# Kernel optimization log

Measured on AMD Instinct MI355X. Metric: run time of the kernel, lower is better.

The kernel has to match this reference:

```python
import jax, jax.numpy as jnp
from jax import lax
import numpy as np

# dims
VOCAB = 64
B, L = 64, 2048
EMB = 128
D_MODEL = 128
N_LAYERS = 4
D_INNER = 256      # expand=2
D_STATE = 16
D_CONV = 4
DT_RANK = 8        # ceil(d_model/16)
NCLS = 3
BN_EPS = 1e-5
RMS_EPS = 1e-5


def setup_inputs():
    key = jax.random.key(0)
    ks = iter(jax.random.split(key, 48))
    def rn(shape, s=0.02):
        return jax.random.normal(next(ks), shape, jnp.float32) * s
    tokens = jax.random.randint(next(ks), (B, L), 0, VOCAB)
    mask = jnp.ones((B, L), jnp.float32)
    emb = rn((VOCAB, EMB)).at[0].set(0.0)  # padding_idx=0
    bn_w = jnp.ones((EMB,), jnp.float32)
    bn_b = jnp.zeros((EMB,), jnp.float32)
    conv_w = rn((D_MODEL, EMB, 3))
    conv_b = jnp.zeros((D_MODEL,), jnp.float32)
    in_proj_w = rn((N_LAYERS, 2 * D_INNER, D_MODEL))
    conv1d_w = rn((N_LAYERS, D_INNER, D_CONV), 0.1)
    conv1d_b = jnp.zeros((N_LAYERS, D_INNER), jnp.float32)
    x_proj_w = rn((N_LAYERS, DT_RANK + 2 * D_STATE, D_INNER))
    dt_proj_w = rn((N_LAYERS, D_INNER, DT_RANK), 0.1)
    dt_proj_b = rn((N_LAYERS, D_INNER), 0.1)
    A_log = jnp.tile(jnp.log(jnp.arange(1, D_STATE + 1, dtype=jnp.float32))[None, None, :],
                     (N_LAYERS, D_INNER, 1))
    D_param = jnp.ones((N_LAYERS, D_INNER), jnp.float32)
    out_proj_w = rn((N_LAYERS, D_MODEL, D_INNER))
    norm_w = jnp.ones((N_LAYERS, D_MODEL), jnp.float32)
    lin1_w = rn((512, D_MODEL)); lin1_b = jnp.zeros((512,), jnp.float32)
    lin2_w = rn((512, 512));     lin2_b = jnp.zeros((512,), jnp.float32)
    lin3_w = rn((NCLS, 512));    lin3_b = jnp.zeros((NCLS,), jnp.float32)
    return dict(tokens=tokens, mask=mask, emb=emb, bn_w=bn_w, bn_b=bn_b,
                conv_w=conv_w, conv_b=conv_b, in_proj_w=in_proj_w,
                conv1d_w=conv1d_w, conv1d_b=conv1d_b, x_proj_w=x_proj_w,
                dt_proj_w=dt_proj_w, dt_proj_b=dt_proj_b, A_log=A_log,
                D_param=D_param, out_proj_w=out_proj_w, norm_w=norm_w,
                lin1_w=lin1_w, lin1_b=lin1_b, lin2_w=lin2_w, lin2_b=lin2_b,
                lin3_w=lin3_w, lin3_b=lin3_b)


def _rmsnorm(x, w):
    return x * lax.rsqrt(jnp.mean(x * x, axis=-1, keepdims=True) + RMS_EPS) * w


def _selective_scan(u, dt, A, Bm, Cm, Dv):
    # u, dt: (B,L,di); A: (di,ds); Bm, Cm: (B,L,ds); Dv: (di,)
    def step(h, inp):
        dt_t, B_t, C_t, u_t = inp           # (B,di),(B,ds),(B,ds),(B,di)
        dA = jnp.exp(dt_t[:, :, None] * A)  # (B,di,ds)
        h = dA * h + (dt_t * u_t)[:, :, None] * B_t[:, None, :]
        y = jnp.einsum('bds,bs->bd', h, C_t)
        return h, y
    h0 = jnp.zeros((u.shape[0], A.shape[0], A.shape[1]), u.dtype)
    xs = (jnp.swapaxes(dt, 0, 1), jnp.swapaxes(Bm, 0, 1),
          jnp.swapaxes(Cm, 0, 1), jnp.swapaxes(u, 0, 1))
    _, ys = lax.scan(step, h0, xs)          # ys: (L,B,di)
    return jnp.swapaxes(ys, 0, 1) + u * Dv


def _mamba(x, in_w, cw, cb, xp_w, dtp_w, dtp_b, A_log, Dv, out_w):
    # x: (B,L,d_model)
    xz = jnp.einsum('bld,ed->ble', x, in_w)            # (B,L,2*di)
    xi, z = jnp.split(xz, 2, axis=-1)
    # causal depthwise conv over time
    xc = jnp.swapaxes(xi, 1, 2)                        # (B,di,L)
    xc = lax.conv_general_dilated(xc, cw[:, None, :], (1,), [(D_CONV - 1, 0)],
                                  dimension_numbers=('NCH', 'OIH', 'NCH'),
                                  feature_group_count=D_INNER)
    xc = jax.nn.silu(xc + cb[None, :, None])
    xc = jnp.swapaxes(xc, 1, 2)                        # (B,L,di)
    x_dbl = jnp.einsum('bld,ed->ble', xc, xp_w)        # (B,L,dtr+2*ds)
    dt = jax.nn.softplus(jnp.einsum('blr,dr->bld', x_dbl[..., :DT_RANK], dtp_w) + dtp_b)
    Bm = x_dbl[..., DT_RANK:DT_RANK + D_STATE]
    Cm = x_dbl[..., DT_RANK + D_STATE:]
    A = -jnp.exp(A_log)                                # (di,ds)
    y = _selective_scan(xc, dt, A, Bm, Cm, Dv)
    y = y * jax.nn.silu(z)
    return jnp.einsum('ble,de->bld', y, out_w)         # (B,L,d_model)


def _forward(tokens, mask, emb, bn_w, bn_b, conv_w, conv_b, in_proj_w,
             conv1d_w, conv1d_b, x_proj_w, dt_proj_w, dt_proj_b, A_log,
             D_param, out_proj_w, norm_w, lin1_w, lin1_b, lin2_w, lin2_b,
             lin3_w, lin3_b):
    x = emb[tokens]                                    # (B,L,E)
    xc = jnp.swapaxes(x, 1, 2)                         # (B,E,L)
    # BatchNorm1d in eval mode: running_mean=0, running_var=1
    xc = xc * (bn_w * lax.rsqrt(jnp.array(1.0 + BN_EPS)))[None, :, None] + bn_b[None, :, None]
    xc = lax.conv_general_dilated(xc, conv_w, (1,), [(1, 1)],
                                  dimension_numbers=('NCH', 'OIH', 'NCH'))
    xc = jax.nn.relu(xc + conv_b[None, :, None])
    x = jnp.swapaxes(xc, 1, 2)                         # (B,L,D_MODEL)
    for i in range(N_LAYERS):
        x = _mamba(_rmsnorm(x, norm_w[i]), in_proj_w[i], conv1d_w[i],
                   conv1d_b[i], x_proj_w[i], dt_proj_w[i], dt_proj_b[i],
                   A_log[i], D_param[i], out_proj_w[i]) + x
    # masked average pooling
    m = mask[:, :, None]
    denom = jnp.clip(jnp.sum(m, axis=1), 1e-9, None)   # (B,1)->(B,D) broadcast
    pooled = jnp.sum(x * m, axis=1) / denom
    h = jax.nn.relu(pooled @ lin1_w.T + lin1_b)
    h = jax.nn.relu(h @ lin2_w.T + lin2_b)
    return h @ lin3_w.T + lin3_b                       # (B,NCLS)


def reference(tokens, mask, emb, bn_w, bn_b, conv_w, conv_b, in_proj_w,
              conv1d_w, conv1d_b, x_proj_w, dt_proj_w, dt_proj_b, A_log,
              D_param, out_proj_w, norm_w, lin1_w, lin1_b, lin2_w, lin2_b,
              lin3_w, lin3_b):
    return _forward(tokens, mask, emb, bn_w, bn_b, conv_w, conv_b, in_proj_w,
                    conv1d_w, conv1d_b, x_proj_w, dt_proj_w, dt_proj_b, A_log,
                    D_param, out_proj_w, norm_w, lin1_w, lin1_b, lin2_w,
                    lin2_b, lin3_w, lin3_b)
```

## Files before the change

### kernel.cpp

```cpp
#include <hip/hip_runtime.h>
#include <math.h>

#define NB     64
#define SL     2048
#define NTOK   (NB*SL)
#define EMB_D  128
#define DMODEL 128
#define DIN    256
#define DST    16
#define NLAYER 4
#define SEG    64
#define NSEG   (SL/SEG)
#define L2E    1.4426950408889634f
#define LN2    0.6931471805599453f

typedef __bf16 bf16x8 __attribute__((ext_vector_type(8)));
typedef __bf16 bf16x4 __attribute__((ext_vector_type(4)));
typedef float  f32x4  __attribute__((ext_vector_type(4)));
typedef float  f32x2  __attribute__((ext_vector_type(2)));

#define FIX_PL   ((size_t)0)
#define FIX_PM   (FIX_PL + 131072)
#define FIX_PD   (FIX_PM + 1024)
#define FIX_H1   (FIX_PD + 8192)
#define FIX_H2   (FIX_H1 + 32768)
#define FIX_WP   (FIX_H2 + 32768)
#define FIX_W2B  (FIX_WP + 65536)
#define FIX_WINB (FIX_W2B + 24576)
#define FIX_WOUTB (FIX_WINB + 131072)
#define FIX_END  (FIX_WOUTB + 65536)

__device__ __forceinline__ float fexp2(float x){ return __builtin_amdgcn_exp2f(x); }
__device__ __forceinline__ float flog2(float x){ return __builtin_amdgcn_logf(x); }
__device__ __forceinline__ float frcp (float x){ return __builtin_amdgcn_rcpf(x); }
__device__ __forceinline__ float fast_exp(float x){ return fexp2(x*L2E); }
__device__ __forceinline__ float siluf(float v){ return v * frcp(1.f + fast_exp(-v)); }
__device__ __forceinline__ float softplusf(float a){
  return fmaxf(a,0.f) + flog2(1.f + fexp2(-fabsf(a)*L2E)) * LN2;
}
__device__ __forceinline__ unsigned short bfbits(float x){
  __bf16 b = (__bf16)x; return __builtin_bit_cast(unsigned short, b);
}
__device__ __forceinline__ unsigned int packdu(float dt, float u){
  return ((unsigned int)bfbits(u) << 16) | (unsigned int)bfbits(dt);
}

__device__ __forceinline__ f32x2 pkfma(f32x2 a, f32x2 b, f32x2 c){
#if __has_builtin(__builtin_elementwise_fma)
  return __builtin_elementwise_fma(a, b, c);
#else
  return (f32x2){ fmaf(a.x,b.x,c.x), fmaf(a.y,b.y,c.y) };
#endif
}

__global__ void k_w2b(const float* __restrict__ cw, __bf16* __restrict__ w2){
  int g = blockIdx.x*256 + threadIdx.x;
  if (g >= 128*384) return;
  int d = g / 384, j = g % 384;
  int k = j >> 7, e = j & 127;
  w2[d*384 + k*128 + e] = (__bf16)cw[d*384 + e*3 + k];
}

__global__ void k_cvt(const float* __restrict__ src, __bf16* __restrict__ dst, int n){
  int i = blockIdx.x*256 + threadIdx.x;
  if (i < n) dst[i] = (__bf16)src[i];
}

__global__ void k_wprep(const float* __restrict__ xpw, __bf16* __restrict__ wp){
  int g = blockIdx.x*256 + threadIdx.x;
  int l = g >> 14, rem = g & 16383;
  int n = rem >> 8, k = rem & 255;
  float v = (n < 40) ? xpw[(size_t)l*40*256 + n*256 + k] : 0.f;
  wp[g] = (__bf16)v;
}

__global__ __launch_bounds__(256) void k_rmsscale(const float* __restrict__ x,
                                                  float* __restrict__ rs){
  int wv = threadIdx.x>>6, lane = threadIdx.x&63;
  size_t tok = (size_t)blockIdx.x*4 + wv;
  float2 v = *(const float2*)(x + tok*128 + lane*2);
  float ss = v.x*v.x + v.y*v.y;
  #pragma unroll
  for (int m=1;m<64;m<<=1) ss += __shfl_xor(ss, m);
  float r = rsqrtf(ss*(1.f/128.f) + 1e-5f);
  if (lane == 0) rs[tok] = r;
}

template<int MODE, int K, int N>
__global__ __launch_bounds__(256) void k_mgemm(
    const void* __restrict__ Av, const __bf16* __restrict__ Wb,
    const float* __restrict__ bias, const float* __restrict__ rsp,
    const float* __restrict__ nwp, const float* __restrict__ bnbp,
    float* __restrict__ out, __bf16* __restrict__ outb, __bf16* __restrict__ outz){
  __shared__ __bf16 As[128][40];
  __shared__ __bf16 Bs[128][40];
  const int tid  = threadIdx.x;
  const int wave = tid >> 6;
  const int lane = tid & 63;
  const int col  = lane & 15;
  const int quad = lane >> 4;
  const int wm = (wave & 1) * 64;
  const int wn = (wave >> 1) * 64;
  const int m0 = blockIdx.y * 128;
  const int n0 = blockIdx.x * 128;

  f32x4 acc[4][4];
  #pragma unroll
  for (int i=0;i<4;i++)
    #pragma unroll
    for (int j=0;j<4;j++) acc[i][j] = (f32x4){0.f,0.f,0.f,0.f};

  const int sm = tid >> 3;
  const int sk4 = (tid & 7) * 4;
  const int bn = tid >> 2;
  const int bk8 = (tid & 3) * 8;

  for (int k0 = 0; k0 < K; k0 += 32){
    if constexpr(MODE==0){
      const int* tok = (const int*)Av;
      const int tap = k0 >> 7;
      const int e = (k0 & 127) + sk4;
      const float sc = rsqrtf(1.0f + 1e-5f);
      float4 bw4 = *(const float4*)(nwp + e);
      float4 bb4 = *(const float4*)(bnbp + e);
      float4 s4;
      s4.x = bw4.x*sc; s4.y = bw4.y*sc; s4.z = bw4.z*sc; s4.w = bw4.w*sc;
      #pragma unroll
      for (int p=0;p<4;p++){
        int m = p*32 + sm;
        int tokpos = m0 + m;
        int t = (tokpos & 2047) + tap - 1;
        float4 v = {0.f,0.f,0.f,0.f};
        if ((unsigned)t < 2048u){
          int id = tok[((size_t)(tokpos >> 11) << 11) + t];
          float4 ev = *(const float4*)(rsp + (size_t)id*EMB_D + e);
          v.x = fmaf(ev.x, s4.x, bb4.x);
          v.y = fmaf(ev.y, s4.y, bb4.y);
          v.z = fmaf(ev.z, s4.z, bb4.z);
          v.w = fmaf(ev.w, s4.w, bb4.w);
        }
        bf16x4 o;
        o[0] = (__bf16)v.x; o[1] = (__bf16)v.y; o[2] = (__bf16)v.z; o[3] = (__bf16)v.w;
        *(bf16x4*)&As[m][sk4] = o;
      }
    } else {
      const size_t abase = (size_t)m0 * K;
      #pragma unroll
      for (int p=0;p<4;p++){
        int m = p*32 + sm;
        const float* A = (const float*)Av;
        float4 x4 = *(const float4*)(A + abase + (size_t)m*K + k0 + sk4);
        float4 w4 = *(const float4*)(nwp + k0 + sk4);
        float s = rsp[m0 + m];
        float4 v;
        v.x = x4.x*s*w4.x; v.y = x4.y*s*w4.y; v.z = x4.z*s*w4.z; v.w = x4.w*s*w4.w;
        bf16x4 o;
        o[0] = (__bf16)v.x; o[1] = (__bf16)v.y; o[2] = (__bf16)v.z; o[3] = (__bf16)v.w;
        *(bf16x4*)&As[m][sk4] = o;
      }
    }
    #pragma unroll
    for (int p=0;p<2;p++){
      int n = p*64 + bn;
      bf16x8 w = *(const bf16x8*)(Wb + (size_t)(n0+n)*K + k0 + bk8);
      *(bf16x8*)&Bs[n][bk8] = w;
    }
    __syncthreads();
    bf16x8 af[4], bfr[4];
    const int fq = quad*8;
    #pragma unroll
    for (int i=0;i<4;i++) af[i]  = *(const bf16x8*)&As[wm + i*16 + col][fq];
    #pragma unroll
    for (int j=0;j<4;j++) bfr[j] = *(const bf16x8*)&Bs[wn + j*16 + col][fq];
    #pragma unroll
    for (int i=0;i<4;i++)
      #pragma unroll
      for (int j=0;j<4;j++)
        acc[i][j] = __builtin_amdgcn_mfma_f32_16x16x32_bf16(af[i], bfr[j], acc[i][j], 0, 0, 0);
    __syncthreads();
  }

  #pragma unroll
  for (int i=0;i<4;i++){
    #pragma unroll
    for (int j=0;j<4;j++){
      int n_l = wn + j*16 + col;
      #pragma unroll
      for (int r=0;r<4;r++){
        int m = m0 + wm + i*16 + quad*4 + r;
        float c = acc[i][j][r];
        if constexpr(MODE==0){
          int n = n0 + n_l;
          out[(size_t)m*DMODEL + n] = fmaxf(c + bias[n], 0.f);
        } else {
          int n = n0 + n_l;
          if (n < DIN) outb[(size_t)m*DIN + n]        = (__bf16)c;
          else         outz[(size_t)m*DIN + n - DIN]  = (__bf16)siluf(c);
        }
      }
    }
  }
}

__global__ __launch_bounds__(256) void k_seg(const __bf16* __restrict__ xi,
    const __bf16* __restrict__ wpb,
    const float* __restrict__ cw, const float* __restrict__ cb,
    const float* __restrict__ dtw, const float* __restrict__ dtb,
    const float* __restrict__ alog,
    float* __restrict__ vbc, unsigned int* __restrict__ dub,
    float* __restrict__ cseg, float* __restrict__ sdtb){
  __shared__ __bf16 sxc[64][264];
  __shared__ float vls[64][68];
  const int tid = threadIdx.x;
  const size_t m0 = (size_t)blockIdx.x * 64;
  const int b = (int)(m0 >> 11);
  const int g = (int)((m0 >> 6) & (NSEG-1));
  const int seq0 = (int)(m0 & 2047);

  {
    const int c4 = (tid & 63) * 4;
    const int tw = tid >> 6;
    const int t0 = tw * 16;
    float wc[4][4];
    #pragma unroll
    for (int j=0;j<4;j++)
      #pragma unroll
      for (int k=0;k<4;k++) wc[j][k] = cw[(c4+j)*4 + k];
    float4 cb4 = *(const float4*)(cb + c4);
    bf16x4 zed;
    zed[0] = (__bf16)0.f; zed[1] = (__bf16)0.f; zed[2] = (__bf16)0.f; zed[3] = (__bf16)0.f;
    bf16x4 win[3];
    #pragma unroll
    for (int j=0;j<3;j++){
      int tr = t0 - 3 + j;
      win[j] = (seq0 + tr >= 0) ? *(const bf16x4*)(xi + (m0 + tr)*DIN + c4) : zed;
    }
    #pragma unroll
    for (int i=0;i<16;i++){
      int t = t0 + i;
      bf16x4 w3 = *(const bf16x4*)(xi + (m0 + t)*DIN + c4);
      float4 acc = cb4;
      #pragma unroll
      for (int k=0;k<3;k++){
        acc.x = fmaf(wc[0][k], (float)win[k][0], acc.x);
        acc.y = fmaf(wc[1][k], (float)win[k][1], acc.y);
        acc.z = fmaf(wc[2][k], (float)win[k][2], acc.z);
        acc.w = fmaf(wc[3][k], (float)win[k][3], acc.w);
      }
      acc.x = fmaf(wc[0][3], (float)w3[0], acc.x);
      acc.y = fmaf(wc[1][3], (float)w3[1], acc.y);
      acc.z = fmaf(wc[2][3], (float)w3[2], acc.z);
      acc.w = fmaf(wc[3][3], (float)w3[3], acc.w);
      bf16x4 o;
      o[0]=(__bf16)siluf(acc.x); o[1]=(__bf16)siluf(acc.y);
      o[2]=(__bf16)siluf(acc.z); o[3]=(__bf16)siluf(acc.w);
      *(bf16x4*)&sxc[t][c4] = o;
      win[0] = win[1]; win[1] = win[2]; win[2] = w3;
    }
  }
  __syncthreads();

  {
    const int wave = tid >> 6, lane = tid & 63;
    const int col = lane & 15, quad = lane >> 4;
    const int wn = wave * 16;
    f32x4 acc[4];
    #pragma unroll
    for (int i=0;i<4;i++) acc[i] = (f32x4){0.f,0.f,0.f,0.f};
    #pragma unroll
    for (int kc=0;kc<8;kc++){
      bf16x8 bfr = *(const bf16x8*)(wpb + (size_t)(wn+col)*256 + kc*32 + quad*8);
      #pragma unroll
      for (int mi=0;mi<4;mi++){
        bf16x8 af = *(const bf16x8*)&sxc[mi*16 + col][kc*32 + quad*8];
        acc[mi] = __builtin_amdgcn_mfma_f32_16x16x32_bf16(af, bfr, acc[mi], 0, 0, 0);
      }
    }
    #pragma unroll
    for (int mi=0;mi<4;mi++)
      #pragma unroll
      for (int r=0;r<4;r++)
        vls[mi*16 + quad*4 + r][wn + col] = acc[mi][r];
  }
  __syncthreads();

  #pragma unroll
  for (int p=0;p<8;p++){
    int j = p*256 + tid;
    int t = j >> 5, i = j & 31;
    vbc[(m0+t)*32 + i] = vls[t][8+i];
  }

  {
    const int d = tid;
    const float a0 = -fast_exp(alog[d*DST]) * L2E;
    bool fast = true;
    for (int s=1;s<16;s++){
      float as = -fast_exp(alog[d*DST + s]) * L2E;
      fast = fast && (fabsf(as - (float)(s+1)*a0) <= 1e-3f*fabsf(as));
    }
    float4 w8a = *(const float4*)(dtw + d*8);
    float4 w8b = *(const float4*)(dtw + d*8 + 4);
    const f32x2 wA0 = {w8a.x, w8a.y}, wA1 = {w8a.z, w8a.w};
    const f32x2 wB0 = {w8b.x, w8b.y}, wB1 = {w8b.z, w8b.w};
    const float bd = dtb[d];
    float ssum = 0.f;
    size_t base = (((size_t)b*NSEG + g)*DIN + d)*DST;
    if (fast){
      f32x2 hp[8];
      #pragma unroll
      for (int k=0;k<8;k++) hp[k] = (f32x2){0.f,0.f};
      float4 cv0 = *(const float4*)&vls[0][0];
      float4 cv1 = *(const float4*)&vls[0][4];
      float4 cb0 = *(const float4*)&vls[0][8];
      float4 cb1 = *(const float4*)&vls[0][12];
      float4 cb2 = *(const float4*)&vls[0][16];
      float4 cb3 = *(const float4*)&vls[0][20];
      float cu = (float)sxc[0][d];
      #pragma unroll 2
      for (int t=0;t<SEG;t++){
        float4 v0=cv0, v1=cv1, b0=cb0, b1=cb1, b2=cb2, b3=cb3;
        float u = cu;
        int tn = (t < SEG-1) ? t+1 : SEG-1;
        cv0 = *(const float4*)&vls[tn][0];
        cv1 = *(const float4*)&vls[tn][4];
        cb0 = *(const float4*)&vls[tn][8];
        cb1 = *(const float4*)&vls[tn][12];
        cb2 = *(const float4*)&vls[tn][16];
        cb3 = *(const float4*)&vls[tn][20];
        cu = (float)sxc[tn][d];
        f32x2 la = pkfma((f32x2){v0.x,v0.y}, wA0, (f32x2){bd, 0.f});
        la = pkfma((f32x2){v0.z,v0.w}, wA1, la);
        la = pkfma((f32x2){v1.x,v1.y}, wB0, la);
        la = pkfma((f32x2){v1.z,v1.w}, wB1, la);
        float dt = softplusf(la.x + la.y);
        ssum += dt;
        dub[(m0+t)*DIN + d] = packdu(dt, u);
        float du = dt*u;
        float r1 = fexp2(dt*a0);
        float r2 = r1*r1, r4 = r2*r2, r8 = r4*r4;
        f32x2 p01 = {r1, r2};
        f32x2 s2 = {r2, r2}, s4 = {r4, r4}, s8 = {r8, r8};
        f32x2 p23 = p01*s2, p45 = p01*s4, p67 = p23*s4;
        f32x2 p89 = p01*s8, pAB = p23*s8, pCD = p45*s8, pEF = p67*s8;
        f32x2 du2 = {du, du};
        hp[0] = pkfma(p01, hp[0], du2*(f32x2){b0.x,b0.y});
        hp[1] = pkfma(p23, hp[1], du2*(f32x2){b0.z,b0.w});
        hp[2] = pkfma(p45, hp[2], du2*(f32x2){b1.x,b1.y});
        hp[3] = pkfma(p67, hp[3], du2*(f32x2){b1.z,b1.w});
        hp[4] = pkfma(p89, hp[4], du2*(f32x2){b2.x,b2.y});
        hp[5] = pkfma(pAB, hp[5], du2*(f32x2){b2.z,b2.w});
        hp[6] = pkfma(pCD, hp[6], du2*(f32x2){b3.x,b3.y});
        hp[7] = pkfma(pEF, hp[7], du2*(f32x2){b3.z,b3.w});
      }
      #pragma unroll
      for (int k=0;k<4;k++){
        float4 o = { hp[2*k].x, hp[2*k].y, hp[2*k+1].x, hp[2*k+1].y };
        *(float4*)(cseg + base + 4*k) = o;
      }
    } else {
      float h[16];
      float aA[16];
      #pragma unroll
      for (int k=0;k<16;k++){ h[k] = 0.f; aA[k] = -fast_exp(alog[d*DST + k]) * L2E; }
      for (int t=0;t<SEG;t++){
        float4 v0 = *(const float4*)&vls[t][0];
        float4 v1 = *(const float4*)&vls[t][4];
        float lin = bd;
        lin = fmaf(v0.x,w8a.x, fmaf(v0.y,w8a.y, fmaf(v0.z,w8a.z, fmaf(v0.w,w8a.w, lin))));
        lin = fmaf(v1.x,w8b.x, fmaf(v1.y,w8b.y, fmaf(v1.z,w8b.z, fmaf(v1.w,w8b.w, lin))));
        float dt = softplusf(lin);
        ssum += dt;
        float u = (float)sxc[t][d];
        dub[(m0+t)*DIN + d] = packdu(dt, u);
        float du = dt*u;
        #pragma unroll
        for (int k=0;k<16;k++){
          float e = fexp2(dt*aA[k]);
          h[k] = fmaf(e, h[k], du*vls[t][8+k]);
        }
      }
      #pragma unroll
      for (int k=0;k<4;k++){
        float4 o = { h[4*k], h[4*k+1], h[4*k+2], h[4*k+3] };
        *(float4*)(cseg + base + 4*k) = o;
      }
    }
    sdtb[((size_t)b*NSEG + g)*DIN + d] = ssum;
  }
}

__global__ __launch_bounds__(256) void k_scanB(float* __restrict__ cseg,
    const float* __restrict__ sdtb, const float* __restrict__ alog){
  int gl = blockIdx.x*256 + threadIdx.x;
  int b   = gl >> 12;
  int rem = gl & 4095;
  int d = rem >> 4, s = rem & 15;
  const float a = -fast_exp(alog[d*DST + s]) * L2E;
  float cvals[NSEG];
  float sdv[NSEG];
  #pragma unroll
  for (int g=0; g<NSEG; g++){
    size_t base = ((size_t)b*NSEG + g)*DIN;
    sdv[g]   = sdtb[base + d];
    cvals[g] = cseg[(base + d)*DST + s];
  }
  float h = 0.f;
  #pragma unroll
  for (int g=0; g<NSEG; g++){
    size_t ci = (((size_t)b*NSEG + g)*DIN + d)*DST + s;
    cseg[ci] = h;
    h = fmaf(fexp2(a*sdv[g]), h, cvals[g]);
  }
}

__global__ __launch_bounds__(256) void k_scanC3(float* __restrict__ xres,
    const unsigned int* __restrict__ dub, const float* __restrict__ vbc,
    const __bf16* __restrict__ gzb,
    const float* __restrict__ alog, const float* __restrict__ Dpar,
    const float* __restrict__ cseg, const __bf16* __restrict__ wout,
    float* __restrict__ rs){
  __shared__ __bf16 sy[64][264];
  __shared__ float svbc[64][32];
  float* sx = (float*)sy;
  const int tid = threadIdx.x;
  const size_t m0 = (size_t)blockIdx.x * 64;
  const int b = (int)(m0 >> 11);
  const int g = (int)((m0 >> 6) & (NSEG-1));

  #pragma unroll
  for (int p=0;p<8;p++){
    int j = p*256 + tid;
    int t = j >> 5, i = j & 31;
    svbc[t][i] = vbc[(m0+t)*32 + i];
  }

  {
    const int d = tid;
    const float a0 = -fast_exp(alog[d*DST]) * L2E;
    bool fast = true;
    for (int s=1;s<16;s++){
      float as = -fast_exp(alog[d*DST + s]) * L2E;
      fast = fast && (fabsf(as - (float)(s+1)*a0) <= 1e-3f*fabsf(as));
    }
    const float Dv = Dpar[d];
    size_t base = (((size_t)b*NSEG + g)*DIN + d)*DST;
    float4 hv0 = *(const float4*)(cseg + base);
    float4 hv1 = *(const float4*)(cseg + base + 4);
    float4 hv2 = *(const float4*)(cseg + base + 8);
    float4 hv3 = *(const float4*)(cseg + base + 12);
    __syncthreads();

    if (fast){
      f32x2 hp[8] = { {hv0.x,hv0.y},{hv0.z,hv0.w},{hv1.x,hv1.y},{hv1.z,hv1.w},
                      {hv2.x,hv2.y},{hv2.z,hv2.w},{hv3.x,hv3.y},{hv3.z,hv3.w} };

#define LOADCH(WV,GV,T0) \
      _Pragma("unroll") \
      for (int q=0;q<8;q++){ \
        WV[q] = dub[(m0 + (T0) + q)*DIN + d]; \
        GV[q] = gzb[(m0 + (T0) + q)*DIN + d]; \
      }

#define SCSTEP(T,WW,GG) { \
      int Tn = ((T) < SEG-1) ? (T)+1 : SEG-1; \
      float4 nb0 = *(const float4*)&svbc[Tn][0]; \
      float4 nb1 = *(const float4*)&svbc[Tn][4]; \
      float4 nb2 = *(const float4*)&svbc[Tn][8]; \
      float4 nb3 = *(const float4*)&svbc[Tn][12]; \
      float4 nb4 = *(const float4*)&svbc[Tn][16]; \
      float4 nb5 = *(const float4*)&svbc[Tn][20]; \
      float4 nb6 = *(const float4*)&svbc[Tn][24]; \
      float4 nb7 = *(const float4*)&svbc[Tn][28]; \
      float u  = __builtin_bit_cast(float, (WW) & 0xffff0000u); \
      float dt = __builtin_bit_cast(float, (WW) << 16); \
      float du = dt*u; \
      float r1 = fexp2(dt*a0); \
      float r2 = r1*r1, r4 = r2*r2, r8 = r4*r4; \
      f32x2 p01 = {r1, r2}; \
      f32x2 s2 = {r2, r2}, s4 = {r4, r4}, s8 = {r8, r8}; \
      f32x2 p23 = p01*s2, p45 = p01*s4, p67 = p23*s4; \
      f32x2 p89 = p01*s8, pAB = p23*s8, pCD = p45*s8, pEF = p67*s8; \
      f32x2 du2 = {du, du}; \
      f32x2 ya = {0.f,0.f}, yb = {0.f,0.f}; \
      hp[0] = pkfma(p01, hp[0], du2*(f32x2){pb0.x,pb0.y}); \
      ya = pkfma(hp[0], (f32x2){pb4.x,pb4.y}, ya); \
      hp[1] = pkfma(p23, hp[1], du2*(f32x2){pb0.z,pb0.w}); \
      yb = pkfma(hp[1], (f32x2){pb4.z,pb4.w}, yb); \
      hp[2] = pkfma(p45, hp[2], du2*(f32x2){pb1.x,pb1.y}); \
      ya = pkfma(hp[2], (f32x2){pb5.x,pb5.y}, ya); \
      hp[3] = pkfma(p67, hp[3], du2*(f32x2){pb1.z,pb1.w}); \
      yb = pkfma(hp[3], (f32x2){pb5.z,pb5.w}, yb); \
      hp[4] = pkfma(p89, hp[4], du2*(f32x2){pb2.x,pb2.y}); \
      ya = pkfma(hp[4], (f32x2){pb6.x,pb6.y}, ya); \
      hp[5] = pkfma(pAB, hp[5], du2*(f32x2){pb2.z,pb2.w}); \
      yb = pkfma(hp[5], (f32x2){pb6.z,pb6.w}, yb); \
      hp[6] = pkfma(pCD, hp[6], du2*(f32x2){pb3.x,pb3.y}); \
      ya = pkfma(hp[6], (f32x2){pb7.x,pb7.y}, ya); \
      hp[7] = pkfma(pEF, hp[7], du2*(f32x2){pb3.z,pb3.w}); \
      yb = pkfma(hp[7], (f32x2){pb7.z,pb7.w}, yb); \
      f32x2 ys = ya + yb; \
      float y = ys.x + ys.y; \
      sy[T][d] = (__bf16)((y + u*Dv) * (float)(GG)); \
      pb0=nb0; pb1=nb1; pb2=nb2; pb3=nb3; pb4=nb4; pb5=nb5; pb6=nb6; pb7=nb7; }

      unsigned int wv0[8], wv1[8];
      __bf16 gv0[8], gv1[8];
      LOADCH(wv0, gv0, 0)
      float4 pb0 = *(const float4*)&svbc[0][0];
      float4 pb1 = *(const float4*)&svbc[0][4];
      float4 pb2 = *(const float4*)&svbc[0][8];
      float4 pb3 = *(const float4*)&svbc[0][12];
      float4 pb4 = *(const float4*)&svbc[0][16];
      float4 pb5 = *(const float4*)&svbc[0][20];
      float4 pb6 = *(const float4*)&svbc[0][24];
      float4 pb7 = *(const float4*)&svbc[0][28];
      #pragma unroll
      for (int tc=0; tc<SEG; tc+=16){
        LOADCH(wv1, gv1, tc+8)
        #pragma unroll
        for (int q=0;q<8;q++){ SCSTEP(tc+q, wv0[q], gv0[q]) }
        if (tc+16 < SEG){ LOADCH(wv0, gv0, tc+16) }
        #pragma unroll
        for (int q=0;q<8;q++){ SCSTEP(tc+8+q, wv1[q], gv1[q]) }
      }
#undef LOADCH
#undef SCSTEP
    } else {
      float h[16] = {hv0.x,hv0.y,hv0.z,hv0.w, hv1.x,hv1.y,hv1.z,hv1.w,
                     hv2.x,hv2.y,hv2.z,hv2.w, hv3.x,hv3.y,hv3.z,hv3.w};
      float aA[16];
      #pragma unroll
      for (int k=0;k<16;k++) aA[k] = -fast_exp(alog[d*DST + k]) * L2E;
      for (int t=0;t<SEG;t++){
        unsigned int w = dub[(m0+t)*DIN + d];
        float u  = __builtin_bit_cast(float, w & 0xffff0000u);
        float dt = __builtin_bit_cast(float, w << 16);
        float du = dt*u;
        float y = 0.f;
        #pragma unroll
        for (int k=0;k<16;k++){
          float e = fexp2(dt*aA[k]);
          h[k] = fmaf(e, h[k], du*svbc[t][k]);
          y = fmaf(h[k], svbc[t][16+k], y);
        }
        float gz = (float)gzb[(m0+t)*DIN + d];
        sy[t][d] = (__bf16)((y + u*Dv) * gz);
      }
    }
  }
  __syncthreads();

  const int wave = tid >> 6, lane = tid & 63;
  const int col = lane & 15, quad = lane >> 4;
  const int wn = wave * 32;
  f32x4 acc[4][2];
  #pragma unroll
  for (int i=0;i<4;i++)
    #pragma unroll
    for (int j=0;j<2;j++) acc[i][j] = (f32x4){0.f,0.f,0.f,0.f};
  #pragma unroll
  for (int kc=0;kc<8;kc++){
    bf16x8 bfr0 = *(const bf16x8*)(wout + (size_t)(wn +      col)*256 + kc*32 + quad*8);
    bf16x8 bfr1 = *(const bf16x8*)(wout + (size_t)(wn + 16 + col)*256 + kc*32 + quad*8);
    #pragma unroll
    for (int mi=0;mi<4;mi++){
      bf16x8 af = *(const bf16x8*)&sy[mi*16 + col][kc*32 + quad*8];
      acc[mi][0] = __builtin_amdgcn_mfma_f32_16x16x32_bf16(af, bfr0, acc[mi][0], 0, 0, 0);
      acc[mi][1] = __builtin_amdgcn_mfma_f32_16x16x32_bf16(af, bfr1, acc[mi][1], 0, 0, 0);
    }
  }
  __syncthreads();

  #pragma unroll
  for (int mi=0;mi<4;mi++){
    #pragma unroll
    for (int j=0;j<2;j++){
      int n = wn + j*16 + col;
      #pragma unroll
      for (int r=0;r<4;r++){
        int ml = mi*16 + quad*4 + r;
        size_t go = (m0 + ml)*DMODEL + n;
        float nx = xres[go] + acc[mi][j][r];
        xres[go] = nx;
        sx[ml*132 + n] = nx;
      }
    }
  }
  __syncthreads();
  {
    int row = tid >> 2, q = tid & 3;
    const float* pr = sx + row*132 + q*32;
    float ss = 0.f;
    #pragma unroll
    for (int i=0;i<32;i+=4){
      float4 v = *(const float4*)(pr + i);
      ss += v.x*v.x + v.y*v.y + v.z*v.z + v.w*v.w;
    }
    ss += __shfl_xor(ss, 1);
    ss += __shfl_xor(ss, 2);
    if (q == 0) rs[m0 + row] = rsqrtf(ss*(1.f/128.f) + 1e-5f);
  }
}

__global__ __launch_bounds__(256) void k_pool1(const float* __restrict__ x,
    const float* __restrict__ mask, float* __restrict__ part, float* __restrict__ pmask){
  int b = blockIdx.y, seg = blockIdx.x;
  int d = threadIdx.x & 127, half = threadIdx.x >> 7;
  int t0 = seg*128 + half*64;
  float acc = 0.f, macc = 0.f;
  for (int i=0;i<64;i++){
    int t = t0 + i;
    float mv = mask[(size_t)b*SL + t];
    acc = fmaf(x[((size_t)b*SL + t)*DMODEL + d], mv, acc);
    macc += mv;
  }
  __shared__ float sm[256];
  __shared__ float smm[2];
  sm[threadIdx.x] = acc;
  if (d == 0) smm[half] = macc;
  __syncthreads();
  if (half == 0){
    part[((size_t)b*16 + seg)*128 + d] = sm[d] + sm[128+d];
    if (d == 0) pmask[b*16 + seg] = smm[0] + smm[1];
  }
}

__global__ __launch_bounds__(512) void k_head(const float* __restrict__ part,
    const float* __restrict__ pmask,
    const float* __restrict__ l1w, const float* __restrict__ l1b,
    const float* __restrict__ l2w, const float* __restrict__ l2b,
    const float* __restrict__ l3w, const float* __restrict__ l3b,
    float* __restrict__ out){
  __shared__ float sp[128];
  __shared__ float sh[512];
  int b = blockIdx.x, tid = threadIdx.x;
  if (tid < 128){
    float acc = 0.f, ms = 0.f;
    for (int s=0;s<16;s++){
      acc += part[((size_t)b*16+s)*128 + tid];
      ms  += pmask[b*16+s];
    }
    sp[tid] = acc / fmaxf(ms, 1e-9f);
  }
  __syncthreads();
  {
    const float4* pw = (const float4*)(l1w + (size_t)tid*128);
    const float4* pi = (const float4*)sp;
    float acc = 0.f;
    #pragma unroll 8
    for (int k=0;k<32;k++){
      float4 a = pi[k], w = pw[k];
      acc = fmaf(a.x,w.x, fmaf(a.y,w.y, fmaf(a.z,w.z, fmaf(a.w,w.w, acc))));
    }
    __syncthreads();
    sh[tid] = fmaxf(acc + l1b[tid], 0.f);
  }
  __syncthreads();
  float h2v;
  {
    const float4* pw = (const float4*)(l2w + (size_t)tid*512);
    const float4* pi = (const float4*)sh;
    float acc = 0.f;
    #pragma unroll 8
    for (int k=0;k<128;k++){
      float4 a = pi[k], w = pw[k];
      acc = fmaf(a.x,w.x, fmaf(a.y,w.y, fmaf(a.z,w.z, fmaf(a.w,w.w, acc))));
    }
    h2v = fmaxf(acc + l2b[tid], 0.f);
  }
  __syncthreads();
  sh[tid] = h2v;
  __syncthreads();
  if (tid < 192){
    int n = tid >> 6, lane = tid & 63;
    float acc = 0.f;
    for (int k=lane; k<512; k+=64) acc = fmaf(sh[k], l3w[(size_t)n*512+k], acc);
    #pragma unroll
    for (int m=1;m<64;m<<=1) acc += __shfl_xor(acc, m);
    if (lane == 0) out[(size_t)b*3 + n] = acc + l3b[n];
  }
}

extern "C" void kernel_launch(void* const* d_in, const int* in_sizes, int n_in,
                              void* d_out, int out_size, void* d_ws, size_t ws_size,
                              hipStream_t stream){
  const int*   tokens = (const int*)  d_in[0];
  const float* mask   = (const float*)d_in[1];
  const float* emb    = (const float*)d_in[2];
  const float* bn_w   = (const float*)d_in[3];
  const float* bn_b   = (const float*)d_in[4];
  const float* conv_w = (const float*)d_in[5];
  const float* conv_b = (const float*)d_in[6];
  const float* in_w   = (const float*)d_in[7];
  const float* c1_w   = (const float*)d_in[8];
  const float* c1_b   = (const float*)d_in[9];
  const float* xp_w   = (const float*)d_in[10];
  const float* dtp_w  = (const float*)d_in[11];
  const float* dtp_b  = (const float*)d_in[12];
  const float* A_log  = (const float*)d_in[13];
  const float* D_par  = (const float*)d_in[14];
  const float* out_w  = (const float*)d_in[15];
  const float* nrm_w  = (const float*)d_in[16];
  const float* l1w = (const float*)d_in[17]; const float* l1b = (const float*)d_in[18];
  const float* l2w = (const float*)d_in[19]; const float* l2b = (const float*)d_in[20];
  const float* l3w = (const float*)d_in[21]; const float* l3b = (const float*)d_in[22];
  float* dout = (float*)d_out;

  int CB = 64;
  while (CB > 1 && ((size_t)CB*SL*741 + FIX_END)*4 > ws_size) CB >>= 1;
  if (((size_t)CB*SL*741 + FIX_END)*4 > ws_size) return;
  const size_t CTOK = (size_t)CB*SL;

  float* ws  = (float*)d_ws;
  float* pl  = ws + FIX_PL;
  float* pm  = ws + FIX_PM;
  __bf16* wpb   = (__bf16*)(ws + FIX_WP);
  __bf16* w2b   = (__bf16*)(ws + FIX_W2B);
  __bf16* winb  = (__bf16*)(ws + FIX_WINB);
  __bf16* woutb = (__bf16*)(ws + FIX_WOUTB);
  float* xcb = ws + FIX_END;
  float* rs  = xcb + CTOK*128;
  __bf16* xib = (__bf16*)(rs + CTOK);
  unsigned int* dub = (unsigned int*)(xib + CTOK*256);
  float* vbc = (float*)(dub + CTOK*256);
  float* csg = vbc + CTOK*32;
  float* sdt = csg + CTOK*64;
  __bf16* zb  = (__bf16*)(sdt + CTOK*4);

  k_w2b<<<192, 256, 0, stream>>>(conv_w, w2b);
  k_cvt<<<1024, 256, 0, stream>>>(in_w,  winb,  4*512*128);
  k_cvt<<<512,  256, 0, stream>>>(out_w, woutb, 4*128*256);
  k_wprep<<<256, 256, 0, stream>>>(xp_w, wpb);

  const int nchunks = NB / CB;
  for (int c = 0; c < nchunks; c++){
    const int* tok_c = tokens + (size_t)c*CTOK;

    k_mgemm<0,384,128><<<dim3(1, CTOK/128), 256, 0, stream>>>(
        tok_c, w2b, conv_b, emb, bn_w, bn_b, xcb, nullptr, nullptr);
    k_rmsscale<<<CTOK/4, 256, 0, stream>>>(xcb, rs);

    for (int layer = 0; layer < NLAYER; layer++){
      const __bf16* lin = winb  + (size_t)layer*512*128;
      const float* lcw  = c1_w  + (size_t)layer*DIN*4;
      const float* lcb  = c1_b  + (size_t)layer*DIN;
      const float* ldw  = dtp_w + (size_t)layer*DIN*8;
      const float* ldb  = dtp_b + (size_t)layer*DIN;
      const float* lal  = A_log + (size_t)layer*DIN*DST;
      const float* lD   = D_par + (size_t)layer*DIN;
      const __bf16* low = woutb + (size_t)layer*128*256;
      const float* lnw  = nrm_w + (size_t)layer*128;

      k_mgemm<1,128,512><<<dim3(4, CTOK/128), 256, 0, stream>>>(
          xcb, lin, nullptr, rs, lnw, nullptr, nullptr, xib, zb);
      k_seg<<<(int)(CTOK/64), 256, 0, stream>>>(
          xib, wpb + (size_t)layer*64*256, lcw, lcb, ldw, ldb, lal, vbc, dub, csg, sdt);
      k_scanB<<<CB*16, 256, 0, stream>>>(csg, sdt, lal);
      k_scanC3<<<(int)(CTOK/64), 256, 0, stream>>>(
          xcb, dub, vbc, zb, lal, lD, csg, low, rs);
    }

    k_pool1<<<dim3(16, CB), 256, 0, stream>>>(
        xcb, mask + (size_t)c*CTOK, pl + (size_t)c*CB*16*128, pm + (size_t)c*CB*16);
  }

  k_head<<<NB, 512, 0, stream>>>(pl, pm, l1w, l1b, l2w, l2b, l3w, l3b, dout);
}
```

Baseline: 1.348 ms.

## Split chunked scan output into intra-segment and carried-state parts across kernels

The segment kernel now computes the intra-segment output contribution (C·h from a zero start plus D·u) during its local scan and packs it in bf16 alongside dt. The final kernel then only adds the carried-in state's contribution, using a cumulative-dt decay, instead of re-running the full recurrence. This removes the duplicate recurrence in the final pass and halves the B/C buffer traffic, since only C is stored. The cost is extra work in the first pass and storing the partial output in bf16 rather than u, which may lose precision.

```diff
diff --git a/kernel.cpp b/kernel.cpp
--- a/kernel.cpp
+++ b/kernel.cpp
@@ -41,8 +41,8 @@
 __device__ __forceinline__ unsigned short bfbits(float x){
   __bf16 b = (__bf16)x; return __builtin_bit_cast(unsigned short, b);
 }
-__device__ __forceinline__ unsigned int packdu(float dt, float u){
-  return ((unsigned int)bfbits(u) << 16) | (unsigned int)bfbits(dt);
+__device__ __forceinline__ unsigned int packdu(float dt, float hi){
+  return ((unsigned int)bfbits(hi) << 16) | (unsigned int)bfbits(dt);
 }
 
 __device__ __forceinline__ f32x2 pkfma(f32x2 a, f32x2 b, f32x2 c){
@@ -206,7 +206,7 @@
     const __bf16* __restrict__ wpb,
     const float* __restrict__ cw, const float* __restrict__ cb,
     const float* __restrict__ dtw, const float* __restrict__ dtb,
-    const float* __restrict__ alog,
+    const float* __restrict__ alog, const float* __restrict__ Dpar,
     float* __restrict__ vbc, unsigned int* __restrict__ dub,
     float* __restrict__ cseg, float* __restrict__ sdtb){
   __shared__ __bf16 sxc[64][264];
@@ -285,10 +285,10 @@
   __syncthreads();
 
   #pragma unroll
-  for (int p=0;p<8;p++){
+  for (int p=0;p<4;p++){
     int j = p*256 + tid;
-    int t = j >> 5, i = j & 31;
-    vbc[(m0+t)*32 + i] = vls[t][8+i];
+    int t = j >> 4, i = j & 15;
+    vbc[(m0+t)*16 + i] = vls[t][24+i];
   }
 
   {
@@ -304,6 +304,7 @@
     const f32x2 wA0 = {w8a.x, w8a.y}, wA1 = {w8a.z, w8a.w};
     const f32x2 wB0 = {w8b.x, w8b.y}, wB1 = {w8b.z, w8b.w};
     const float bd = dtb[d];
+    const float Dv = Dpar[d];
     float ssum = 0.f;
     size_t base = (((size_t)b*NSEG + g)*DIN + d)*DST;
     if (fast){
@@ -312,22 +313,32 @@
       for (int k=0;k<8;k++) hp[k] = (f32x2){0.f,0.f};
       float4 cv0 = *(const float4*)&vls[0][0];
       float4 cv1 = *(const float4*)&vls[0][4];
-      float4 cb0 = *(const float4*)&vls[0][8];
-      float4 cb1 = *(const float4*)&vls[0][12];
-      float4 cb2 = *(const float4*)&vls[0][16];
-      float4 cb3 = *(const float4*)&vls[0][20];
+      float4 cbb0 = *(const float4*)&vls[0][8];
+      float4 cbb1 = *(const float4*)&vls[0][12];
+      float4 cbb2 = *(const float4*)&vls[0][16];
+      float4 cbb3 = *(const float4*)&vls[0][20];
+      float4 ccc0 = *(const float4*)&vls[0][24];
+      float4 ccc1 = *(const float4*)&vls[0][28];
+      float4 ccc2 = *(const float4*)&vls[0][32];
+      float4 ccc3 = *(const float4*)&vls[0][36];
       float cu = (float)sxc[0][d];
       #pragma unroll 2
       for (int t=0;t<SEG;t++){
-        float4 v0=cv0, v1=cv1, b0=cb0, b1=cb1, b2=cb2, b3=cb3;
+        float4 v0=cv0, v1=cv1;
+        float4 b0=cbb0, b1=cbb1, b2=cbb2, b3=cbb3;
+        float4 c0=ccc0, c1=ccc1, c2=ccc2, c3=ccc3;
         float u = cu;
         int tn = (t < SEG-1) ? t+1 : SEG-1;
         cv0 = *(const float4*)&vls[tn][0];
         cv1 = *(const float4*)&vls[tn][4];
-        cb0 = *(const float4*)&vls[tn][8];
-        cb1 = *(const float4*)&vls[tn][12];
-        cb2 = *(const float4*)&vls[tn][16];
-        cb3 = *(const float4*)&vls[tn][20];
+        cbb0 = *(const float4*)&vls[tn][8];
+        cbb1 = *(const float4*)&vls[tn][12];
+        cbb2 = *(const float4*)&vls[tn][16];
+        cbb3 = *(const float4*)&vls[tn][20];
+        ccc0 = *(const float4*)&vls[tn][24];
+        ccc1 = *(const float4*)&vls[tn][28];
+        ccc2 = *(const float4*)&vls[tn][32];
+        ccc3 = *(const float4*)&vls[tn][36];
         cu = (float)sxc[tn][d];
         f32x2 la = pkfma((f32x2){v0.x,v0.y}, wA0, (f32x2){bd, 0.f});
         la = pkfma((f32x2){v0.z,v0.w}, wA1, la);
@@ -335,7 +346,6 @@
         la = pkfma((f32x2){v1.z,v1.w}, wB1, la);
         float dt = softplusf(la.x + la.y);
         ssum += dt;
-        dub[(m0+t)*DIN + d] = packdu(dt, u);
         float du = dt*u;
         float r1 = fexp2(dt*a0);
         float r2 = r1*r1, r4 = r2*r2, r8 = r4*r4;
@@ -344,14 +354,26 @@
         f32x2 p23 = p01*s2, p45 = p01*s4, p67 = p23*s4;
         f32x2 p89 = p01*s8, pAB = p23*s8, pCD = p45*s8, pEF = p67*s8;
         f32x2 du2 = {du, du};
+        f32x2 ya = {0.f,0.f}, yb = {0.f,0.f};
         hp[0] = pkfma(p01, hp[0], du2*(f32x2){b0.x,b0.y});
+        ya = pkfma(hp[0], (f32x2){c0.x,c0.y}, ya);
         hp[1] = pkfma(p23, hp[1], du2*(f32x2){b0.z,b0.w});
+        yb = pkfma(hp[1], (f32x2){c0.z,c0.w}, yb);
         hp[2] = pkfma(p45, hp[2], du2*(f32x2){b1.x,b1.y});
+        ya = pkfma(hp[2], (f32x2){c1.x,c1.y}, ya);
         hp[3] = pkfma(p67, hp[3], du2*(f32x2){b1.z,b1.w});
+        yb = pkfma(hp[3], (f32x2){c1.z,c1.w}, yb);
         hp[4] = pkfma(p89, hp[4], du2*(f32x2){b2.x,b2.y});
+        ya = pkfma(hp[4], (f32x2){c2.x,c2.y}, ya);
         hp[5] = pkfma(pAB, hp[5], du2*(f32x2){b2.z,b2.w});
+        yb = pkfma(hp[5], (f32x2){c2.z,c2.w}, yb);
         hp[6] = pkfma(pCD, hp[6], du2*(f32x2){b3.x,b3.y});
+        ya = pkfma(hp[6], (f32x2){c3.x,c3.y}, ya);
         hp[7] = pkfma(pEF, hp[7], du2*(f32x2){b3.z,b3.w});
+        yb = pkfma(hp[7], (f32x2){c3.z,c3.w}, yb);
+        f32x2 ys = ya + yb;
+        float ypart = ys.x + ys.y + u*Dv;
+        dub[(m0+t)*DIN + d] = packdu(dt, ypart);
       }
       #pragma unroll
       for (int k=0;k<4;k++){
@@ -372,13 +394,16 @@
         float dt = softplusf(lin);
         ssum += dt;
         float u = (float)sxc[t][d];
-        dub[(m0+t)*DIN + d] = packdu(dt, u);
         float du = dt*u;
+        float y = 0.f;
         #pragma unroll
         for (int k=0;k<16;k++){
           float e = fexp2(dt*aA[k]);
           h[k] = fmaf(e, h[k], du*vls[t][8+k]);
+          y = fmaf(h[k], vls[t][24+k], y);
         }
+        float ypart = y + u*Dv;
+        dub[(m0+t)*DIN + d] = packdu(dt, ypart);
       }
       #pragma unroll
       for (int k=0;k<4;k++){
@@ -417,11 +442,11 @@
 __global__ __launch_bounds__(256) void k_scanC3(float* __restrict__ xres,
     const unsigned int* __restrict__ dub, const float* __restrict__ vbc,
     const __bf16* __restrict__ gzb,
-    const float* __restrict__ alog, const float* __restrict__ Dpar,
+    const float* __restrict__ alog,
     const float* __restrict__ cseg, const __bf16* __restrict__ wout,
     float* __restrict__ rs){
   __shared__ __bf16 sy[64][264];
-  __shared__ float svbc[64][32];
+  __shared__ float svbc[64][16];
   float* sx = (float*)sy;
   const int tid = threadIdx.x;
   const size_t m0 = (size_t)blockIdx.x * 64;
@@ -429,10 +454,10 @@
   const int g = (int)((m0 >> 6) & (NSEG-1));
 
   #pragma unroll
-  for (int p=0;p<8;p++){
+  for (int p=0;p<4;p++){
     int j = p*256 + tid;
-    int t = j >> 5, i = j & 31;
-    svbc[t][i] = vbc[(m0+t)*32 + i];
+    int t = j >> 4, i = j & 15;
+    svbc[t][i] = vbc[(m0+t)*16 + i];
   }
 
   {
@@ -443,7 +468,6 @@
       float as = -fast_exp(alog[d*DST + s]) * L2E;
       fast = fast && (fabsf(as - (float)(s+1)*a0) <= 1e-3f*fabsf(as));
     }
-    const float Dv = Dpar[d];
     size_t base = (((size_t)b*NSEG + g)*DIN + d)*DST;
     float4 hv0 = *(const float4*)(cseg + base);
     float4 hv1 = *(const float4*)(cseg + base + 4);
@@ -452,8 +476,9 @@
     __syncthreads();
 
     if (fast){
-      f32x2 hp[8] = { {hv0.x,hv0.y},{hv0.z,hv0.w},{hv1.x,hv1.y},{hv1.z,hv1.w},
-                      {hv2.x,hv2.y},{hv2.z,hv2.w},{hv3.x,hv3.y},{hv3.z,hv3.w} };
+      const f32x2 e01={hv0.x,hv0.y}, e23={hv0.z,hv0.w}, e45={hv1.x,hv1.y}, e67={hv1.z,hv1.w};
+      const f32x2 e89={hv2.x,hv2.y}, eAB={hv2.z,hv2.w}, eCD={hv3.x,hv3.y}, eEF={hv3.z,hv3.w};
+      float cum = 0.f;
 
 #define LOADCH(WV,GV,T0) \
       _Pragma("unroll") \
@@ -463,58 +488,35 @@
       }
 
 #define SCSTEP(T,WW,GG) { \
-      int Tn = ((T) < SEG-1) ? (T)+1 : SEG-1; \
-      float4 nb0 = *(const float4*)&svbc[Tn][0]; \
-      float4 nb1 = *(const float4*)&svbc[Tn][4]; \
-      float4 nb2 = *(const float4*)&svbc[Tn][8]; \
-      float4 nb3 = *(const float4*)&svbc[Tn][12]; \
-      float4 nb4 = *(const float4*)&svbc[Tn][16]; \
-      float4 nb5 = *(const float4*)&svbc[Tn][20]; \
-      float4 nb6 = *(const float4*)&svbc[Tn][24]; \
-      float4 nb7 = *(const float4*)&svbc[Tn][28]; \
-      float u  = __builtin_bit_cast(float, (WW) & 0xffff0000u); \
-      float dt = __builtin_bit_cast(float, (WW) << 16); \
-      float du = dt*u; \
-      float r1 = fexp2(dt*a0); \
+      float ypart = __builtin_bit_cast(float, (WW) & 0xffff0000u); \
+      float dt    = __builtin_bit_cast(float, (WW) << 16); \
+      cum += dt; \
+      float r1 = fexp2(cum*a0); \
       float r2 = r1*r1, r4 = r2*r2, r8 = r4*r4; \
       f32x2 p01 = {r1, r2}; \
       f32x2 s2 = {r2, r2}, s4 = {r4, r4}, s8 = {r8, r8}; \
       f32x2 p23 = p01*s2, p45 = p01*s4, p67 = p23*s4; \
       f32x2 p89 = p01*s8, pAB = p23*s8, pCD = p45*s8, pEF = p67*s8; \
-      f32x2 du2 = {du, du}; \
+      float4 c0 = *(const float4*)&svbc[T][0]; \
+      float4 c1 = *(const float4*)&svbc[T][4]; \
+      float4 c2 = *(const float4*)&svbc[T][8]; \
+      float4 c3 = *(const float4*)&svbc[T][12]; \
       f32x2 ya = {0.f,0.f}, yb = {0.f,0.f}; \
-      hp[0] = pkfma(p01, hp[0], du2*(f32x2){pb0.x,pb0.y}); \
-      ya = pkfma(hp[0], (f32x2){pb4.x,pb4.y}, ya); \
-      hp[1] = pkfma(p23, hp[1], du2*(f32x2){pb0.z,pb0.w}); \
-      yb = pkfma(hp[1], (f32x2){pb4.z,pb4.w}, yb); \
-      hp[2] = pkfma(p45, hp[2], du2*(f32x2){pb1.x,pb1.y}); \
-      ya = pkfma(hp[2], (f32x2){pb5.x,pb5.y}, ya); \
-      hp[3] = pkfma(p67, hp[3], du2*(f32x2){pb1.z,pb1.w}); \
-      yb = pkfma(hp[3], (f32x2){pb5.z,pb5.w}, yb); \
-      hp[4] = pkfma(p89, hp[4], du2*(f32x2){pb2.x,pb2.y}); \
-      ya = pkfma(hp[4], (f32x2){pb6.x,pb6.y}, ya); \
-      hp[5] = pkfma(pAB, hp[5], du2*(f32x2){pb2.z,pb2.w}); \
-      yb = pkfma(hp[5], (f32x2){pb6.z,pb6.w}, yb); \
-      hp[6] = pkfma(pCD, hp[6], du2*(f32x2){pb3.x,pb3.y}); \
-      ya = pkfma(hp[6], (f32x2){pb7.x,pb7.y}, ya); \
-      hp[7] = pkfma(pEF, hp[7], du2*(f32x2){pb3.z,pb3.w}); \
-      yb = pkfma(hp[7], (f32x2){pb7.z,pb7.w}, yb); \
+      ya = pkfma(p01*e01, (f32x2){c0.x,c0.y}, ya); \
+      yb = pkfma(p23*e23, (f32x2){c0.z,c0.w}, yb); \
+      ya = pkfma(p45*e45, (f32x2){c1.x,c1.y}, ya); \
+      yb = pkfma(p67*e67, (f32x2){c1.z,c1.w}, yb); \
+      ya = pkfma(p89*e89, (f32x2){c2.x,c2.y}, ya); \
+      yb = pkfma(pAB*eAB, (f32x2){c2.z,c2.w}, yb); \
+      ya = pkfma(pCD*eCD, (f32x2){c3.x,c3.y}, ya); \
+      yb = pkfma(pEF*eEF, (f32x2){c3.z,c3.w}, yb); \
       f32x2 ys = ya + yb; \
-      float y = ys.x + ys.y; \
-      sy[T][d] = (__bf16)((y + u*Dv) * (float)(GG)); \
-      pb0=nb0; pb1=nb1; pb2=nb2; pb3=nb3; pb4=nb4; pb5=nb5; pb6=nb6; pb7=nb7; }
+      float y = ypart + ys.x + ys.y; \
+      sy[T][d] = (__bf16)(y * (float)(GG)); }
 
       unsigned int wv0[8], wv1[8];
       __bf16 gv0[8], gv1[8];
       LOADCH(wv0, gv0, 0)
-      float4 pb0 = *(const float4*)&svbc[0][0];
-      float4 pb1 = *(const float4*)&svbc[0][4];
-      float4 pb2 = *(const float4*)&svbc[0][8];
-      float4 pb3 = *(const float4*)&svbc[0][12];
-      float4 pb4 = *(const float4*)&svbc[0][16];
-      float4 pb5 = *(const float4*)&svbc[0][20];
-      float4 pb6 = *(const float4*)&svbc[0][24];
-      float4 pb7 = *(const float4*)&svbc[0][28];
       #pragma unroll
       for (int tc=0; tc<SEG; tc+=16){
         LOADCH(wv1, gv1, tc+8)
@@ -527,25 +529,23 @@
 #undef LOADCH
 #undef SCSTEP
     } else {
-      float h[16] = {hv0.x,hv0.y,hv0.z,hv0.w, hv1.x,hv1.y,hv1.z,hv1.w,
+      float e[16] = {hv0.x,hv0.y,hv0.z,hv0.w, hv1.x,hv1.y,hv1.z,hv1.w,
                      hv2.x,hv2.y,hv2.z,hv2.w, hv3.x,hv3.y,hv3.z,hv3.w};
       float aA[16];
       #pragma unroll
       for (int k=0;k<16;k++) aA[k] = -fast_exp(alog[d*DST + k]) * L2E;
+      float cum = 0.f;
       for (int t=0;t<SEG;t++){
         unsigned int w = dub[(m0+t)*DIN + d];
-        float u  = __builtin_bit_cast(float, w & 0xffff0000u);
-        float dt = __builtin_bit_cast(float, w << 16);
-        float du = dt*u;
-        float y = 0.f;
+        float ypart = __builtin_bit_cast(float, w & 0xffff0000u);
+        float dt    = __builtin_bit_cast(float, w << 16);
+        cum += dt;
+        float y = ypart;
         #pragma unroll
-        for (int k=0;k<16;k++){
-          float e = fexp2(dt*aA[k]);
-          h[k] = fmaf(e, h[k], du*svbc[t][k]);
-          y = fmaf(h[k], svbc[t][16+k], y);
-        }
+        for (int k=0;k<16;k++)
+          y = fmaf(e[k]*fexp2(aA[k]*cum), svbc[t][k], y);
         float gz = (float)gzb[(m0+t)*DIN + d];
-        sy[t][d] = (__bf16)((y + u*Dv) * gz);
+        sy[t][d] = (__bf16)(y * gz);
       }
     }
   }
@@ -708,8 +708,8 @@
   float* dout = (float*)d_out;
 
   int CB = 64;
-  while (CB > 1 && ((size_t)CB*SL*741 + FIX_END)*4 > ws_size) CB >>= 1;
-  if (((size_t)CB*SL*741 + FIX_END)*4 > ws_size) return;
+  while (CB > 1 && ((size_t)CB*SL*725 + FIX_END)*4 > ws_size) CB >>= 1;
+  if (((size_t)CB*SL*725 + FIX_END)*4 > ws_size) return;
   const size_t CTOK = (size_t)CB*SL;
 
   float* ws  = (float*)d_ws;
@@ -724,7 +724,7 @@
   __bf16* xib = (__bf16*)(rs + CTOK);
   unsigned int* dub = (unsigned int*)(xib + CTOK*256);
   float* vbc = (float*)(dub + CTOK*256);
-  float* csg = vbc + CTOK*32;
+  float* csg = vbc + CTOK*16;
   float* sdt = csg + CTOK*64;
   __bf16* zb  = (__bf16*)(sdt + CTOK*4);
 
@@ -755,10 +755,10 @@
       k_mgemm<1,128,512><<<dim3(4, CTOK/128), 256, 0, stream>>>(
           xcb, lin, nullptr, rs, lnw, nullptr, nullptr, xib, zb);
       k_seg<<<(int)(CTOK/64), 256, 0, stream>>>(
-          xib, wpb + (size_t)layer*64*256, lcw, lcb, ldw, ldb, lal, vbc, dub, csg, sdt);
+          xib, wpb + (size_t)layer*64*256, lcw, lcb, ldw, ldb, lal, lD, vbc, dub, csg, sdt);
       k_scanB<<<CB*16, 256, 0, stream>>>(csg, sdt, lal);
       k_scanC3<<<(int)(CTOK/64), 256, 0, stream>>>(
-          xcb, dub, vbc, zb, lal, lD, csg, low, rs);
+          xcb, dub, vbc, zb, lal, csg, low, rs);
     }
 
     k_pool1<<<dim3(16, CB), 256, 0, stream>>>(
```

Result: slower. 1.439 ms (+6.8%).
